# Optimization experiments

Measured on AMD Instinct MI355X. Metric: run time of the kernel, lower is better.

## Reference

```python
import jax, jax.numpy as jnp
import numpy as np

N = 50000
E = 800000
F_IN = 128


def _gat(h, src, dst, W, a_src, a_dst, bias, heads, out_ch, concat):
    n = h.shape[0]
    z = (h @ W.T).reshape(n, heads, out_ch)              # [N,H,C]
    alpha_s = jnp.sum(z * a_src, axis=-1)                # [N,H]
    alpha_d = jnp.sum(z * a_dst, axis=-1)                # [N,H]
    logits = jax.nn.leaky_relu(alpha_s[src] + alpha_d[dst], 0.2)  # [Etot,H]
    m = jax.ops.segment_max(logits, dst, num_segments=n)
    ex = jnp.exp(logits - m[dst])
    denom = jax.ops.segment_sum(ex, dst, num_segments=n)
    w = ex / (denom[dst] + 1e-16)                        # [Etot,H]
    agg = jax.ops.segment_sum(w[:, :, None] * z[src], dst, num_segments=n)  # [N,H,C]
    if concat:
        out = agg.reshape(n, heads * out_ch)
    else:
        out = agg.mean(axis=1)
    return out + bias


def setup_inputs() -> dict:
    key = jax.random.key(0)
    ks = jax.random.split(key, 16)
    s = lambda *sh: 1.0 / np.sqrt(sh[-1])
    inp = {
        "x": jax.random.normal(ks[0], (N, F_IN), jnp.float32),
        "edge_index": jax.random.randint(ks[1], (2, E), 0, N, jnp.int64),
        # GraphConv(no_node_features=128 -> 128, aggr='add')
        "W_rel": jax.random.normal(ks[2], (128, F_IN), jnp.float32) * s(128, F_IN),
        "b_rel": jnp.zeros((128,), jnp.float32),
        "W_root": jax.random.normal(ks[3], (128, F_IN), jnp.float32) * s(128, F_IN),
        # GATConv(128 -> 8, heads=8, concat) => 64
        "W1": jax.random.normal(ks[4], (64, 128), jnp.float32) * s(64, 128),
        "a1_src": jax.random.normal(ks[5], (8, 8), jnp.float32) * 0.35,
        "a1_dst": jax.random.normal(ks[6], (8, 8), jnp.float32) * 0.35,
        "b1": jnp.zeros((64,), jnp.float32),
        # GATConv(64 -> 64, heads=1, concat=False)
        "W2": jax.random.normal(ks[7], (64, 64), jnp.float32) * s(64, 64),
        "a2_src": jax.random.normal(ks[8], (1, 64), jnp.float32) * 0.125,
        "a2_dst": jax.random.normal(ks[9], (1, 64), jnp.float32) * 0.125,
        "b2": jnp.zeros((64,), jnp.float32),
        "Wr": jax.random.normal(ks[10], (1, 64), jnp.float32) * s(1, 64),
        "br": jnp.zeros((1,), jnp.float32),
    }
    return inp


def reference(x, edge_index, W_rel, b_rel, W_root, W1, a1_src, a1_dst, b1,
              W2, a2_src, a2_dst, b2, Wr, br):
    src, dst = edge_index[0], edge_index[1]
    # GraphConv, aggr='add': W_rel @ sum_{j in N(i)} x_j + b + W_root @ x_i
    nbr = jax.ops.segment_sum(x[src], dst, num_segments=N)
    h = nbr @ W_rel.T + b_rel + x @ W_root.T
    h = jax.nn.elu(h)
    # GATConv adds self-loops by default
    loop = jnp.arange(N, dtype=edge_index.dtype)
    src2 = jnp.concatenate([src, loop])
    dst2 = jnp.concatenate([dst, loop])
    h = _gat(h, src2, dst2, W1, a1_src, a1_dst, b1, heads=8, out_ch=8, concat=True)
    h = jax.nn.elu(h)
    h = _gat(h, src2, dst2, W2, a2_src, a2_dst, b2, heads=1, out_ch=64, concat=False)
    # final 'mean' aggregation over all nodes (single graph)
    g = jnp.mean(h, axis=0, keepdims=True)               # [1,64]
    return g @ Wr.T + br                                  # [1,1]
```

## Files before the change

kernel.cpp:

```cpp
#include <hip/hip_runtime.h>
#include <hip/hip_bf16.h>
#include <math.h>

#define N_NODES 50000
#define N_EDGES 800000
#define F_IN 128
#define NBUCK 391
#define EPB 4096
#define NBB 196

typedef __attribute__((ext_vector_type(8))) short bf16x8;
typedef __attribute__((ext_vector_type(4))) float f32x4;
typedef __attribute__((ext_vector_type(2))) float f32x2;
typedef unsigned long long ull;

__device__ __forceinline__ float elu_f(float x)   { return x > 0.f ? x : expm1f(x); }
__device__ __forceinline__ float lrelu_f(float x) { return x > 0.f ? x : 0.2f * x; }
__device__ __forceinline__ int   clampN(int v)    { return v < 0 ? 0 : (v >= N_NODES ? N_NODES - 1 : v); }
__device__ __forceinline__ float bits2f(unsigned int u) { union { unsigned int u; float f; } x; x.u = u; return x.f; }
__device__ __forceinline__ float bf2f(unsigned short s) { return bits2f(((unsigned int)s) << 16); }
__device__ __forceinline__ unsigned short f2bfbits(float f) {
    __hip_bfloat16 b = __float2bfloat16(f);
    return __builtin_bit_cast(unsigned short, b);
}
__device__ __forceinline__ unsigned int pack2(float lo, float hi) {
    return ((unsigned int)f2bfbits(hi) << 16) | f2bfbits(lo);
}

#define CAST_X_IDS (N_NODES * 32)
#define CAST_IDS (CAST_X_IDS + 32768 + 8192 + 4096)
#define CASTB ((CAST_IDS + 255) / 256)
__global__ __launch_bounds__(256) void k_prep(const int* __restrict__ dst,
                                              const float* __restrict__ x,
                                              const float* __restrict__ W_rel,
                                              const float* __restrict__ W_root,
                                              const float* __restrict__ W1,
                                              const float* __restrict__ W2,
                                              int* __restrict__ part,
                                              __hip_bfloat16* __restrict__ Abuf,
                                              unsigned int* __restrict__ x8,
                                              __hip_bfloat16* __restrict__ Wc,
                                              __hip_bfloat16* __restrict__ W1b,
                                              __hip_bfloat16* __restrict__ W2b,
                                              float* __restrict__ red,
                                              int* __restrict__ done) {
    __shared__ int hist[NBUCK];
    int tid = threadIdx.x;
    if (blockIdx.x < NBB) {
        for (int j = tid; j < NBUCK; j += 256) hist[j] = 0;
        __syncthreads();
        int base = blockIdx.x * EPB;
        #pragma unroll
        for (int t = 0; t < EPB / 256; ++t) {
            int e = base + t * 256 + tid;
            if (e < N_EDGES) atomicAdd(&hist[clampN(dst[e]) >> 7], 1);
        }
        __syncthreads();
        for (int j = tid; j < NBUCK; j += 256)
            part[(size_t)blockIdx.x * NBUCK + j] = hist[j];
    } else {
        if (blockIdx.x == NBB) {
            red[tid] = 0.f;
            if (tid == 0) done[0] = 0;
        }
        int id = (blockIdx.x - NBB) * 256 + tid;
        if (id < CAST_X_IDS) {
            int i = id >> 5, c4 = (id & 31) * 4;
            float4 v = *(const float4*)&x[(size_t)i * 128 + c4];
            ull p = (ull)f2bfbits(v.x) | ((ull)f2bfbits(v.y) << 16)
                  | ((ull)f2bfbits(v.z) << 32) | ((ull)f2bfbits(v.w) << 48);
            *(ull*)&Abuf[(size_t)i * 256 + 128 + c4] = p;
            int t = __builtin_amdgcn_cvt_pk_fp8_f32(v.x, v.y, 0, false);
            t = __builtin_amdgcn_cvt_pk_fp8_f32(v.z, v.w, t, true);
            x8[(size_t)i * 32 + (id & 31)] = (unsigned int)t;
        } else if (id < CAST_IDS) {
            int j = id - CAST_X_IDS;
            if (j < 32768) {
                int cc = j >> 8, k = j & 255;
                float v = (k < 128) ? W_rel[cc * 128 + k] : W_root[cc * 128 + (k - 128)];
                Wc[j] = __float2bfloat16(v);
            } else if (j < 32768 + 8192) {
                W1b[j - 32768] = __float2bfloat16(W1[j - 32768]);
            } else {
                W2b[j - 32768 - 8192] = __float2bfloat16(W2[j - 32768 - 8192]);
            }
        }
    }
}

__global__ __launch_bounds__(512) void k_bscan(const int* __restrict__ part,
                                               int* __restrict__ boff,
                                               int* __restrict__ bcur) {
    __shared__ int wsum[8];
    __shared__ int wbase[8];
    int tid = threadIdx.x;
    int lane = tid & 63, wid = tid >> 6;
    int v = 0;
    if (tid < NBUCK) {
        for (int b = 0; b < NBB; ++b) v += part[(size_t)b * NBUCK + tid];
    }
    int x = v;
    #pragma unroll
    for (int d = 1; d < 64; d <<= 1) {
        int t = __shfl_up(x, d, 64);
        if (lane >= d) x += t;
    }
    if (lane == 63) wsum[wid] = x;
    __syncthreads();
    if (tid == 0) {
        int b = 0;
        #pragma unroll
        for (int w = 0; w < 8; ++w) { wbase[w] = b; b += wsum[w]; }
    }
    __syncthreads();
    if (tid < NBUCK) {
        int e = wbase[wid] + x - v;
        boff[tid] = e;
        bcur[tid] = e;
    }
    if (tid == 0) boff[NBUCK] = N_EDGES;
}

__global__ __launch_bounds__(256) void k_bscatter(const int* __restrict__ src,
                                                  const int* __restrict__ dst,
                                                  int* __restrict__ bcur,
                                                  unsigned int* __restrict__ ebuf) {
    __shared__ int hist[NBUCK];
    __shared__ int hbase[NBUCK];
    int tid = threadIdx.x;
    for (int j = tid; j < NBUCK; j += 256) hist[j] = 0;
    __syncthreads();
    int base = blockIdx.x * EPB;
    unsigned int myP[EPB / 256]; int myB[EPB / 256], myR[EPB / 256];
    #pragma unroll
    for (int t = 0; t < EPB / 256; ++t) {
        int e = base + t * 256 + tid;
        if (e < N_EDGES) {
            int d = clampN(dst[e]);
            int s = clampN(src[e]);
            myP[t] = ((unsigned int)s << 7) | (unsigned int)(d & 127);
            myB[t] = d >> 7;
            myR[t] = atomicAdd(&hist[d >> 7], 1);
        } else myB[t] = -1;
    }
    __syncthreads();
    for (int j = tid; j < NBUCK; j += 256)
        if (hist[j]) hbase[j] = atomicAdd(&bcur[j], hist[j]);
    __syncthreads();
    #pragma unroll
    for (int t = 0; t < EPB / 256; ++t) {
        if (myB[t] >= 0) ebuf[hbase[myB[t]] + myR[t]] = myP[t];
    }
}

__global__ __launch_bounds__(256) void k_bfinal(const unsigned int* __restrict__ ebuf,
                                                const int* __restrict__ boff,
                                                int* __restrict__ offsets,
                                                int* __restrict__ csr) {
    __shared__ int cnt[128];
    __shared__ int cur[128];
    __shared__ int ws[4];
    int b = blockIdx.x;
    int tid = threadIdx.x;
    int node0 = b << 7;
    int k0 = boff[b], k1 = boff[b + 1];
    if (tid < 128) cnt[tid] = 0;
    __syncthreads();
    for (int k = k0 + tid; k < k1; k += 256)
        atomicAdd(&cnt[ebuf[k] & 127u], 1);
    __syncthreads();
    int lane = tid & 63;
    int v = (tid < 128) ? cnt[tid] : 0;
    int x = v;
    #pragma unroll
    for (int d = 1; d < 64; d <<= 1) {
        int t = __shfl_up(x, d, 64);
        if (lane >= d) x += t;
    }
    if (lane == 63) ws[tid >> 6] = x;
    __syncthreads();
    if (tid < 128) {
        int add = (tid >> 6) ? ws[0] : 0;
        int excl = k0 + add + x - v;
        cur[tid] = excl;
        int node = node0 + tid;
        if (node < N_NODES) offsets[node] = excl;
    }
    if (b == NBUCK - 1 && tid == 0) offsets[N_NODES] = N_EDGES;
    __syncthreads();
    for (int k = k0 + tid; k < k1; k += 256) {
        unsigned int e = ebuf[k];
        int r = atomicAdd(&cur[e & 127u], 1);
        csr[r] = (int)(e >> 7);
    }
}

__global__ __launch_bounds__(256) void k_gather(const unsigned int* __restrict__ x8,
                                                const int* __restrict__ offsets,
                                                const int* __restrict__ csr,
                                                ull* __restrict__ outNbr) {
    int i = blockIdx.x * 8 + (threadIdx.x >> 5);
    int l = threadIdx.x & 31;
    int k0 = offsets[i], k1 = offsets[i + 1];
    float a0 = 0.f, a1 = 0.f, a2 = 0.f, a3 = 0.f;
    for (int kb = k0; kb < k1; kb += 8) {
        int s[8]; int vm[8];
        #pragma unroll
        for (int j = 0; j < 8; ++j) {
            int kk = kb + j;
            vm[j] = kk < k1;
            s[j] = csr[vm[j] ? kk : k1 - 1];
        }
        unsigned int u[8];
        #pragma unroll
        for (int j = 0; j < 8; ++j) u[j] = x8[(size_t)s[j] * 32 + l];
        #pragma unroll
        for (int j = 0; j < 8; ++j) {
            if (vm[j]) {
                f32x2 lo = __builtin_amdgcn_cvt_pk_f32_fp8(u[j], false);
                f32x2 hi = __builtin_amdgcn_cvt_pk_f32_fp8(u[j], true);
                a0 += lo.x; a1 += lo.y; a2 += hi.x; a3 += hi.y;
            }
        }
    }
    outNbr[(size_t)i * 64 + l] = (ull)pack2(a0, a1) | ((ull)pack2(a2, a3) << 32);
}

__global__ __launch_bounds__(256) void k_gemm12(const __hip_bfloat16* __restrict__ A,
                                                const __hip_bfloat16* __restrict__ Wc,
                                                const float* __restrict__ bias,
                                                const __hip_bfloat16* __restrict__ W1b,
                                                const float* __restrict__ a_src,
                                                const float* __restrict__ a_dst,
                                                float* __restrict__ as_o,
                                                float* __restrict__ ad_o,
                                                unsigned int* __restrict__ z8) {
    __shared__ __align__(16) short smem[64 * 136];
    short (*sA)[40] = (short(*)[40])smem;
    short (*sW)[40] = (short(*)[40])(smem + 64 * 40);
    int tid = threadIdx.x;
    int lane = tid & 63, wave = tid >> 6;
    int quad = lane >> 4, l16 = lane & 15;
    int node0 = blockIdx.x * 64;
    int srow = tid >> 2, schk = (tid & 3) * 8;
    int ga = node0 + srow; if (ga >= N_NODES) ga = N_NODES - 1;
    const short* Ap = (const short*)A + (size_t)ga * 256 + schk;
    const short* Wp = (const short*)Wc;
    f32x4 acc[8];
    #pragma unroll
    for (int t = 0; t < 8; ++t) acc[t] = (f32x4){0.f, 0.f, 0.f, 0.f};
    for (int k0 = 0; k0 < 256; k0 += 32) {
        *(bf16x8*)&sA[srow][schk] = *(const bf16x8*)(Ap + k0);
        #pragma unroll
        for (int it = 0; it < 2; ++it) {
            int wrow = srow + it * 64;
            *(bf16x8*)&sW[wrow][schk] = *(const bf16x8*)(Wp + (size_t)wrow * 256 + k0 + schk);
        }
        __syncthreads();
        bf16x8 a = *(const bf16x8*)&sA[wave * 16 + l16][quad * 8];
        #pragma unroll
        for (int nt = 0; nt < 8; ++nt) {
            bf16x8 b = *(const bf16x8*)&sW[nt * 16 + l16][quad * 8];
            acc[nt] = __builtin_amdgcn_mfma_f32_16x16x32_bf16(a, b, acc[nt], 0, 0, 0);
        }
        __syncthreads();
    }
    #pragma unroll
    for (int nt = 0; nt < 8; ++nt) {
        int col = nt * 16 + l16;
        float bv = bias[col];
        #pragma unroll
        for (int r = 0; r < 4; ++r) {
            int row = wave * 16 + quad * 4 + r;
            smem[row * 136 + col] = (short)f2bfbits(elu_f(acc[nt][r] + bv));
        }
    }
    __syncthreads();
    f32x4 acc2[4];
    #pragma unroll
    for (int t = 0; t < 4; ++t) acc2[t] = (f32x4){0.f, 0.f, 0.f, 0.f};
    const short* W1p = (const short*)W1b;
    #pragma unroll
    for (int k0 = 0; k0 < 128; k0 += 32) {
        bf16x8 a = *(const bf16x8*)&smem[(wave * 16 + l16) * 136 + k0 + quad * 8];
        #pragma unroll
        for (int nt = 0; nt < 4; ++nt) {
            bf16x8 b = *(const bf16x8*)(W1p + (size_t)(nt * 16 + l16) * 128 + k0 + quad * 8);
            acc2[nt] = __builtin_amdgcn_mfma_f32_16x16x32_bf16(a, b, acc2[nt], 0, 0, 0);
        }
    }
    __syncthreads();
    #pragma unroll
    for (int nt = 0; nt < 4; ++nt) {
        int col = nt * 16 + l16;
        #pragma unroll
        for (int r = 0; r < 4; ++r) {
            int row = wave * 16 + quad * 4 + r;
            smem[row * 72 + col] = (short)f2bfbits(acc2[nt][r]);
        }
    }
    __syncthreads();
    int row = tid >> 2, chunk = tid & 3;
    int gi = node0 + row;
    float v[16];
    bf16x8 c0 = *(const bf16x8*)&smem[row * 72 + chunk * 16];
    bf16x8 c1 = *(const bf16x8*)&smem[row * 72 + chunk * 16 + 8];
    #pragma unroll
    for (int j = 0; j < 8; ++j) {
        v[j]     = bf2f((unsigned short)c0[j]);
        v[8 + j] = bf2f((unsigned short)c1[j]);
    }
    float ps0 = 0.f, pd0 = 0.f, ps1 = 0.f, pd1 = 0.f;
    #pragma unroll
    for (int j = 0; j < 8; ++j) {
        ps0 += v[j] * a_src[chunk * 16 + j];
        pd0 += v[j] * a_dst[chunk * 16 + j];
        ps1 += v[8 + j] * a_src[chunk * 16 + 8 + j];
        pd1 += v[8 + j] * a_dst[chunk * 16 + 8 + j];
    }
    if (gi < N_NODES) {
        as_o[(size_t)gi * 8 + 2 * chunk]     = ps0;
        as_o[(size_t)gi * 8 + 2 * chunk + 1] = ps1;
        ad_o[(size_t)gi * 8 + 2 * chunk]     = pd0;
        ad_o[(size_t)gi * 8 + 2 * chunk + 1] = pd1;
        #pragma unroll
        for (int wi = 0; wi < 4; ++wi) {
            int t = __builtin_amdgcn_cvt_pk_fp8_f32(v[4 * wi], v[4 * wi + 1], 0, false);
            t = __builtin_amdgcn_cvt_pk_fp8_f32(v[4 * wi + 2], v[4 * wi + 3], t, true);
            z8[(size_t)gi * 16 + chunk * 4 + wi] = (unsigned int)t;
        }
    }
}

__global__ __launch_bounds__(256) void k_gat1z2(const unsigned int* __restrict__ z8,
                                                const float* __restrict__ as1,
                                                const float* __restrict__ ad1,
                                                const float* __restrict__ b1,
                                                const int* __restrict__ offsets,
                                                const int* __restrict__ csr,
                                                const __hip_bfloat16* __restrict__ W2b,
                                                const float* __restrict__ a2s,
                                                const float* __restrict__ a2d,
                                                const float* __restrict__ Wr,
                                                float* __restrict__ as2,
                                                float* __restrict__ ad2,
                                                float* __restrict__ zr) {
    __shared__ __align__(16) short sH2[16 * 72];
    __shared__ __align__(16) short sZ2[16 * 72];
    int iloc = threadIdx.x >> 4;
    int i = blockIdx.x * 16 + iloc;
    int l = threadIdx.x & 15;
    int hd = l >> 1;
    int wh = l & 7, slot = l >> 3;
    int k0 = offsets[i], k1 = offsets[i + 1];
    float ad_h = ad1[(size_t)i * 8 + hd];
    float adw  = ad1[(size_t)i * 8 + wh];
    float e_self = __expf(lrelu_f(as1[(size_t)i * 8 + hd] + ad_h));
    unsigned int uz = z8[(size_t)i * 16 + l];
    f32x2 zlo = __builtin_amdgcn_cvt_pk_f32_fp8(uz, false);
    f32x2 zhi = __builtin_amdgcn_cvt_pk_f32_fp8(uz, true);
    float acc0 = e_self * zlo.x, acc1 = e_self * zlo.y;
    float acc2 = e_self * zhi.x, acc3 = e_self * zhi.y;
    float denp = 0.f;
    for (int kb = k0; kb < k1; kb += 8) {
        int sr[4]; float er[4];
        #pragma unroll
        for (int m = 0; m < 4; ++m) {
            int kk = kb + 2 * m + slot;
            bool v = kk < k1;
            int s = csr[v ? kk : k1 - 1];
            sr[m] = s;
            er[m] = v ? __expf(lrelu_f(as1[(size_t)s * 8 + wh] + adw)) : 0.f;
            denp += er[m];
        }
        int sj[8]; float ej[8]; unsigned int u[8];
        #pragma unroll
        for (int m = 0; m < 4; ++m) {
            #pragma unroll
            for (int sb = 0; sb < 2; ++sb) {
                sj[2 * m + sb] = __shfl(sr[m], sb * 8 + hd, 16);
                ej[2 * m + sb] = __shfl(er[m], sb * 8 + hd, 16);
            }
        }
        #pragma unroll
        for (int j = 0; j < 8; ++j) u[j] = z8[(size_t)sj[j] * 16 + l];
        #pragma unroll
        for (int j = 0; j < 8; ++j) {
            f32x2 alo = __builtin_amdgcn_cvt_pk_f32_fp8(u[j], false);
            f32x2 ahi = __builtin_amdgcn_cvt_pk_f32_fp8(u[j], true);
            acc0 += ej[j] * alo.x; acc1 += ej[j] * alo.y;
            acc2 += ej[j] * ahi.x; acc3 += ej[j] * ahi.y;
        }
    }
    denp += __shfl_xor(denp, 8, 16);
    float den = __shfl(denp, hd, 16) + e_self;
    float inv = 1.f / den;
    float r0 = elu_f(acc0 * inv + b1[4 * l + 0]);
    float r1 = elu_f(acc1 * inv + b1[4 * l + 1]);
    float r2 = elu_f(acc2 * inv + b1[4 * l + 2]);
    float r3 = elu_f(acc3 * inv + b1[4 * l + 3]);
    *(ull*)&sH2[iloc * 72 + 4 * l] = (ull)pack2(r0, r1) | ((ull)pack2(r2, r3) << 32);
    __syncthreads();
    int lane = threadIdx.x & 63, wave = threadIdx.x >> 6;
    int quad = lane >> 4, l16 = lane & 15;
    f32x4 accz = (f32x4){0.f, 0.f, 0.f, 0.f};
    const short* W2p = (const short*)W2b;
    #pragma unroll
    for (int kk0 = 0; kk0 < 64; kk0 += 32) {
        bf16x8 a = *(const bf16x8*)&sH2[l16 * 72 + kk0 + quad * 8];
        bf16x8 b = *(const bf16x8*)(W2p + (size_t)(wave * 16 + l16) * 64 + kk0 + quad * 8);
        accz = __builtin_amdgcn_mfma_f32_16x16x32_bf16(a, b, accz, 0, 0, 0);
    }
    #pragma unroll
    for (int r = 0; r < 4; ++r)
        sZ2[(quad * 4 + r) * 72 + wave * 16 + l16] = (short)f2bfbits(accz[r]);
    __syncthreads();
    ull pz = *(const ull*)&sZ2[iloc * 72 + 4 * l];
    float v0 = bf2f((unsigned short)(pz & 0xffff));
    float v1 = bf2f((unsigned short)((pz >> 16) & 0xffff));
    float v2 = bf2f((unsigned short)((pz >> 32) & 0xffff));
    float v3 = bf2f((unsigned short)(pz >> 48));
    float ps = v0 * a2s[4 * l + 0] + v1 * a2s[4 * l + 1] + v2 * a2s[4 * l + 2] + v3 * a2s[4 * l + 3];
    float pd = v0 * a2d[4 * l + 0] + v1 * a2d[4 * l + 1] + v2 * a2d[4 * l + 2] + v3 * a2d[4 * l + 3];
    float pr = v0 * Wr[4 * l + 0]  + v1 * Wr[4 * l + 1]  + v2 * Wr[4 * l + 2]  + v3 * Wr[4 * l + 3];
    #pragma unroll
    for (int d = 8; d >= 1; d >>= 1) {
        ps += __shfl_xor(ps, d, 16);
        pd += __shfl_xor(pd, d, 16);
        pr += __shfl_xor(pr, d, 16);
    }
    if (l == 0) { as2[i] = ps; ad2[i] = pd; zr[i] = pr; }
}

__global__ __launch_bounds__(256) void k_gat2s(const float* __restrict__ zr,
                                               const float* __restrict__ as2,
                                               const float* __restrict__ ad2,
                                               const int* __restrict__ offsets,
                                               const int* __restrict__ csr,
                                               const float* __restrict__ b2,
                                               const float* __restrict__ Wr,
                                               const float* __restrict__ br,
                                               float* __restrict__ red,
                                               int* __restrict__ done,
                                               float* __restrict__ out) {
    __shared__ float wsum[4];
    __shared__ int lastFlag;
    int tid = threadIdx.x;
    int n = blockIdx.x * 64 + (tid >> 2);
    int r = tid & 3;
    float c = 0.f;
    if (n < N_NODES) {
        int k0 = offsets[n], k1 = offsets[n + 1];
        float ad = ad2[n];
        float den = 0.f, num = 0.f;
        for (int k = k0 + r; k < k1; k += 4) {
            int s = csr[k];
            float e = __expf(lrelu_f(as2[s] + ad));
            den += e;
            num += e * zr[s];
        }
        den += __shfl_xor(den, 1, 64); den += __shfl_xor(den, 2, 64);
        num += __shfl_xor(num, 1, 64); num += __shfl_xor(num, 2, 64);
        if (r == 0) {
            float es = __expf(lrelu_f(as2[n] + ad));
            den += es;
            num += es * zr[n];
            c = num / den;
        }
    }
    #pragma unroll
    for (int d = 4; d <= 32; d <<= 1) c += __shfl_xor(c, d, 64);
    int lane = tid & 63, wave = tid >> 6;
    if (lane == 0) wsum[wave] = c;
    __syncthreads();
    if (tid == 0) {
        float s = wsum[0] + wsum[1] + wsum[2] + wsum[3];
        atomicAdd(&red[blockIdx.x & 255], s);
        __threadfence();
        int old = atomicAdd(done, 1);
        lastFlag = (old == (int)gridDim.x - 1);
    }
    __syncthreads();
    if (lastFlag) {
        __threadfence();
        if (tid < 64) {
            float rv = atomicAdd(&red[tid], 0.f) + atomicAdd(&red[tid + 64], 0.f)
                     + atomicAdd(&red[tid + 128], 0.f) + atomicAdd(&red[tid + 192], 0.f);
            float p = rv * (1.0f / N_NODES) + b2[tid] * Wr[tid];
            #pragma unroll
            for (int d = 32; d >= 1; d >>= 1) p += __shfl_xor(p, d, 64);
            if (tid == 0) out[0] = p + br[0];
        }
    }
}

extern "C" void kernel_launch(void* const* d_in, const int* in_sizes, int n_in,
                              void* d_out, int out_size, void* d_ws, size_t ws_size,
                              hipStream_t stream) {
    const float* x      = (const float*)d_in[0];
    const int*   edges  = (const int*)d_in[1];
    const float* W_rel  = (const float*)d_in[2];
    const float* b_rel  = (const float*)d_in[3];
    const float* W_root = (const float*)d_in[4];
    const float* W1     = (const float*)d_in[5];
    const float* a1s    = (const float*)d_in[6];
    const float* a1d    = (const float*)d_in[7];
    const float* b1     = (const float*)d_in[8];
    const float* W2     = (const float*)d_in[9];
    const float* a2s    = (const float*)d_in[10];
    const float* a2d    = (const float*)d_in[11];
    const float* b2     = (const float*)d_in[12];
    const float* Wr     = (const float*)d_in[13];
    const float* br     = (const float*)d_in[14];
    float* out = (float*)d_out;

    const int* src = edges;
    const int* dst = edges + N_EDGES;

    char* ws = (char*)d_ws;
    size_t p = 0;
    auto alloc = [&](size_t bytes) -> void* {
        void* r = ws + p;
        p = (p + bytes + 255) & ~(size_t)255;
        return r;
    };
    int*   part    = (int*)alloc((size_t)NBB * NBUCK * 4);
    int*   boff    = (int*)alloc((size_t)(NBUCK + 1) * 4);
    int*   bcur    = (int*)alloc((size_t)NBUCK * 4);
    unsigned int* ebuf = (unsigned int*)alloc((size_t)N_EDGES * 4);
    int*   offsets = (int*)alloc((size_t)(N_NODES + 1) * 4);
    int*   csr     = (int*)alloc((size_t)N_EDGES * 4);
    __hip_bfloat16* Abuf = (__hip_bfloat16*)alloc((size_t)N_NODES * 256 * 2);
    unsigned int* x8 = (unsigned int*)alloc((size_t)N_NODES * 32 * 4);
    __hip_bfloat16* Wc   = (__hip_bfloat16*)alloc((size_t)128 * 256 * 2);
    __hip_bfloat16* W1b  = (__hip_bfloat16*)alloc((size_t)64 * 128 * 2);
    __hip_bfloat16* W2b  = (__hip_bfloat16*)alloc((size_t)64 * 64 * 2);
    float* as1 = (float*)alloc((size_t)N_NODES * 8 * 4);
    float* ad1 = (float*)alloc((size_t)N_NODES * 8 * 4);
    float* as2 = (float*)alloc((size_t)N_NODES * 4);
    float* ad2 = (float*)alloc((size_t)N_NODES * 4);
    float* zr  = (float*)alloc((size_t)N_NODES * 4);
    unsigned int* z1e8 = (unsigned int*)alloc((size_t)N_NODES * 16 * 4);
    float* red = (float*)alloc(256 * 4);
    int*   done = (int*)alloc(4);

    const int MB   = (N_NODES + 63) / 64;
    const int NB8  = N_NODES / 8;
    const int NB16 = N_NODES / 16;

    k_prep    <<<NBB + CASTB, 256, 0, stream>>>(dst, x, W_rel, W_root, W1, W2,
                                                part, Abuf, x8, Wc, W1b, W2b, red, done);
    k_bscan   <<<1, 512, 0, stream>>>(part, boff, bcur);
    k_bscatter<<<NBB, 256, 0, stream>>>(src, dst, bcur, ebuf);
    k_bfinal  <<<NBUCK, 256, 0, stream>>>(ebuf, boff, offsets, csr);
    k_gather  <<<NB8, 256, 0, stream>>>(x8, offsets, csr, (ull*)Abuf);
    k_gemm12  <<<MB, 256, 0, stream>>>(Abuf, Wc, b_rel, W1b, a1s, a1d, as1, ad1, z1e8);
    k_gat1z2  <<<NB16, 256, 0, stream>>>(z1e8, as1, ad1, b1, offsets, csr,
                                         W2b, a2s, a2d, Wr, as2, ad2, zr);
    k_gat2s   <<<MB, 256, 0, stream>>>(zr, as2, ad2, offsets, csr, b2, Wr, br,
                                       red, done, out);
}
```

Baseline: 235.8 us.

## Use fixed-capacity buckets, drop histogram/scan, fuse neighbor gather into GEMM kernel

Replaces the histogram-plus-scan bucket sort with fixed-capacity buckets (CAP slots per 128-node bucket) addressed through a global counter, removing the histogram pass and the single-block scan kernel. Node offsets become int2 (begin,end) pairs because the CSR is no longer contiguous. The neighbor-sum gather now runs inside the GEMM kernel and writes straight into shared memory, so the bf16 neighbor half of Abuf is no longer written to and reread from global memory. The cost is a bucket that overflows if more than CAP edges land in it, and less parallelism in the fused gather phase.

```diff
diff --git a/kernel.cpp b/kernel.cpp
--- a/kernel.cpp
+++ b/kernel.cpp
@@ -8,6 +8,8 @@
 #define NBUCK 391
 #define EPB 4096
 #define NBB 196
+#define CAP 4096
+#define APITCH 264
 
 typedef __attribute__((ext_vector_type(8))) short bf16x8;
 typedef __attribute__((ext_vector_type(4))) float f32x4;
@@ -30,100 +32,53 @@
 #define CAST_X_IDS (N_NODES * 32)
 #define CAST_IDS (CAST_X_IDS + 32768 + 8192 + 4096)
 #define CASTB ((CAST_IDS + 255) / 256)
-__global__ __launch_bounds__(256) void k_prep(const int* __restrict__ dst,
-                                              const float* __restrict__ x,
+__global__ __launch_bounds__(256) void k_prep(const float* __restrict__ x,
                                               const float* __restrict__ W_rel,
                                               const float* __restrict__ W_root,
                                               const float* __restrict__ W1,
                                               const float* __restrict__ W2,
-                                              int* __restrict__ part,
                                               __hip_bfloat16* __restrict__ Abuf,
                                               unsigned int* __restrict__ x8,
                                               __hip_bfloat16* __restrict__ Wc,
                                               __hip_bfloat16* __restrict__ W1b,
                                               __hip_bfloat16* __restrict__ W2b,
+                                              int* __restrict__ gcount,
                                               float* __restrict__ red,
                                               int* __restrict__ done) {
-    __shared__ int hist[NBUCK];
     int tid = threadIdx.x;
-    if (blockIdx.x < NBB) {
-        for (int j = tid; j < NBUCK; j += 256) hist[j] = 0;
-        __syncthreads();
-        int base = blockIdx.x * EPB;
-        #pragma unroll
-        for (int t = 0; t < EPB / 256; ++t) {
-            int e = base + t * 256 + tid;
-            if (e < N_EDGES) atomicAdd(&hist[clampN(dst[e]) >> 7], 1);
-        }
-        __syncthreads();
-        for (int j = tid; j < NBUCK; j += 256)
-            part[(size_t)blockIdx.x * NBUCK + j] = hist[j];
-    } else {
-        if (blockIdx.x == NBB) {
-            red[tid] = 0.f;
-            if (tid == 0) done[0] = 0;
-        }
-        int id = (blockIdx.x - NBB) * 256 + tid;
-        if (id < CAST_X_IDS) {
-            int i = id >> 5, c4 = (id & 31) * 4;
-            float4 v = *(const float4*)&x[(size_t)i * 128 + c4];
-            ull p = (ull)f2bfbits(v.x) | ((ull)f2bfbits(v.y) << 16)
-                  | ((ull)f2bfbits(v.z) << 32) | ((ull)f2bfbits(v.w) << 48);
-            *(ull*)&Abuf[(size_t)i * 256 + 128 + c4] = p;
-            int t = __builtin_amdgcn_cvt_pk_fp8_f32(v.x, v.y, 0, false);
-            t = __builtin_amdgcn_cvt_pk_fp8_f32(v.z, v.w, t, true);
-            x8[(size_t)i * 32 + (id & 31)] = (unsigned int)t;
-        } else if (id < CAST_IDS) {
-            int j = id - CAST_X_IDS;
-            if (j < 32768) {
-                int cc = j >> 8, k = j & 255;
-                float v = (k < 128) ? W_rel[cc * 128 + k] : W_root[cc * 128 + (k - 128)];
-                Wc[j] = __float2bfloat16(v);
-            } else if (j < 32768 + 8192) {
-                W1b[j - 32768] = __float2bfloat16(W1[j - 32768]);
-            } else {
-                W2b[j - 32768 - 8192] = __float2bfloat16(W2[j - 32768 - 8192]);
-            }
-        }
-    }
-}
-
-__global__ __launch_bounds__(512) void k_bscan(const int* __restrict__ part,
-                                               int* __restrict__ boff,
-                                               int* __restrict__ bcur) {
-    __shared__ int wsum[8];
-    __shared__ int wbase[8];
-    int tid = threadIdx.x;
-    int lane = tid & 63, wid = tid >> 6;
-    int v = 0;
-    if (tid < NBUCK) {
-        for (int b = 0; b < NBB; ++b) v += part[(size_t)b * NBUCK + tid];
-    }
-    int x = v;
-    #pragma unroll
-    for (int d = 1; d < 64; d <<= 1) {
-        int t = __shfl_up(x, d, 64);
-        if (lane >= d) x += t;
-    }
-    if (lane == 63) wsum[wid] = x;
-    __syncthreads();
-    if (tid == 0) {
-        int b = 0;
-        #pragma unroll
-        for (int w = 0; w < 8; ++w) { wbase[w] = b; b += wsum[w]; }
-    }
-    __syncthreads();
-    if (tid < NBUCK) {
-        int e = wbase[wid] + x - v;
-        boff[tid] = e;
-        bcur[tid] = e;
-    }
-    if (tid == 0) boff[NBUCK] = N_EDGES;
+    if (blockIdx.x == 0) {
+        red[tid] = 0.f;
+        if (tid < NBUCK) gcount[tid] = 0;
+        if (tid + 256 < NBUCK) gcount[tid + 256] = 0;
+        if (tid == 0) done[0] = 0;
+    }
+    int id = blockIdx.x * 256 + tid;
+    if (id < CAST_X_IDS) {
+        int i = id >> 5, c4 = (id & 31) * 4;
+        float4 v = *(const float4*)&x[(size_t)i * 128 + c4];
+        ull p = (ull)f2bfbits(v.x) | ((ull)f2bfbits(v.y) << 16)
+              | ((ull)f2bfbits(v.z) << 32) | ((ull)f2bfbits(v.w) << 48);
+        *(ull*)&Abuf[(size_t)i * 128 + c4] = p;
+        int t = __builtin_amdgcn_cvt_pk_fp8_f32(v.x, v.y, 0, false);
+        t = __builtin_amdgcn_cvt_pk_fp8_f32(v.z, v.w, t, true);
+        x8[(size_t)i * 32 + (id & 31)] = (unsigned int)t;
+    } else if (id < CAST_IDS) {
+        int j = id - CAST_X_IDS;
+        if (j < 32768) {
+            int cc = j >> 8, k = j & 255;
+            float v = (k < 128) ? W_rel[cc * 128 + k] : W_root[cc * 128 + (k - 128)];
+            Wc[j] = __float2bfloat16(v);
+        } else if (j < 32768 + 8192) {
+            W1b[j - 32768] = __float2bfloat16(W1[j - 32768]);
+        } else {
+            W2b[j - 32768 - 8192] = __float2bfloat16(W2[j - 32768 - 8192]);
+        }
+    }
 }
 
 __global__ __launch_bounds__(256) void k_bscatter(const int* __restrict__ src,
                                                   const int* __restrict__ dst,
-                                                  int* __restrict__ bcur,
+                                                  int* __restrict__ gcount,
                                                   unsigned int* __restrict__ ebuf) {
     __shared__ int hist[NBUCK];
     __shared__ int hbase[NBUCK];
@@ -145,7 +100,7 @@
     }
     __syncthreads();
     for (int j = tid; j < NBUCK; j += 256)
-        if (hist[j]) hbase[j] = atomicAdd(&bcur[j], hist[j]);
+        if (hist[j]) hbase[j] = j * CAP + atomicAdd(&gcount[j], hist[j]);
     __syncthreads();
     #pragma unroll
     for (int t = 0; t < EPB / 256; ++t) {
@@ -154,8 +109,8 @@
 }
 
 __global__ __launch_bounds__(256) void k_bfinal(const unsigned int* __restrict__ ebuf,
-                                                const int* __restrict__ boff,
-                                                int* __restrict__ offsets,
+                                                const int* __restrict__ gcount,
+                                                int2* __restrict__ offs,
                                                 int* __restrict__ csr) {
     __shared__ int cnt[128];
     __shared__ int cur[128];
@@ -163,7 +118,7 @@
     int b = blockIdx.x;
     int tid = threadIdx.x;
     int node0 = b << 7;
-    int k0 = boff[b], k1 = boff[b + 1];
+    int k0 = b * CAP, k1 = k0 + gcount[b];
     if (tid < 128) cnt[tid] = 0;
     __syncthreads();
     for (int k = k0 + tid; k < k1; k += 256)
@@ -184,9 +139,8 @@
         int excl = k0 + add + x - v;
         cur[tid] = excl;
         int node = node0 + tid;
-        if (node < N_NODES) offsets[node] = excl;
-    }
-    if (b == NBUCK - 1 && tid == 0) offsets[N_NODES] = N_EDGES;
+        if (node < N_NODES) offs[node] = make_int2(excl, excl + v);
+    }
     __syncthreads();
     for (int k = k0 + tid; k < k1; k += 256) {
         unsigned int e = ebuf[k];
@@ -195,38 +149,10 @@
     }
 }
 
-__global__ __launch_bounds__(256) void k_gather(const unsigned int* __restrict__ x8,
-                                                const int* __restrict__ offsets,
+__global__ __launch_bounds__(256) void k_gemm12(const unsigned int* __restrict__ x8,
+                                                const int2* __restrict__ offs,
                                                 const int* __restrict__ csr,
-                                                ull* __restrict__ outNbr) {
-    int i = blockIdx.x * 8 + (threadIdx.x >> 5);
-    int l = threadIdx.x & 31;
-    int k0 = offsets[i], k1 = offsets[i + 1];
-    float a0 = 0.f, a1 = 0.f, a2 = 0.f, a3 = 0.f;
-    for (int kb = k0; kb < k1; kb += 8) {
-        int s[8]; int vm[8];
-        #pragma unroll
-        for (int j = 0; j < 8; ++j) {
-            int kk = kb + j;
-            vm[j] = kk < k1;
-            s[j] = csr[vm[j] ? kk : k1 - 1];
-        }
-        unsigned int u[8];
-        #pragma unroll
-        for (int j = 0; j < 8; ++j) u[j] = x8[(size_t)s[j] * 32 + l];
-        #pragma unroll
-        for (int j = 0; j < 8; ++j) {
-            if (vm[j]) {
-                f32x2 lo = __builtin_amdgcn_cvt_pk_f32_fp8(u[j], false);
-                f32x2 hi = __builtin_amdgcn_cvt_pk_f32_fp8(u[j], true);
-                a0 += lo.x; a1 += lo.y; a2 += hi.x; a3 += hi.y;
-            }
-        }
-    }
-    outNbr[(size_t)i * 64 + l] = (ull)pack2(a0, a1) | ((ull)pack2(a2, a3) << 32);
-}
-
-__global__ __launch_bounds__(256) void k_gemm12(const __hip_bfloat16* __restrict__ A,
+                                                const __hip_bfloat16* __restrict__ Ax,
                                                 const __hip_bfloat16* __restrict__ Wc,
                                                 const float* __restrict__ bias,
                                                 const __hip_bfloat16* __restrict__ W1b,
@@ -235,29 +161,69 @@
                                                 float* __restrict__ as_o,
                                                 float* __restrict__ ad_o,
                                                 unsigned int* __restrict__ z8) {
-    __shared__ __align__(16) short smem[64 * 136];
-    short (*sA)[40] = (short(*)[40])smem;
-    short (*sW)[40] = (short(*)[40])(smem + 64 * 40);
+    __shared__ __align__(16) short smem[64 * APITCH + 128 * 40];
+    short* sAF = smem;
+    short (*sW)[40] = (short(*)[40])(smem + 64 * APITCH);
     int tid = threadIdx.x;
     int lane = tid & 63, wave = tid >> 6;
     int quad = lane >> 4, l16 = lane & 15;
     int node0 = blockIdx.x * 64;
+
+    {
+        int l = tid & 31;
+        for (int r8 = 0; r8 < 8; ++r8) {
+            int rloc = r8 * 8 + (tid >> 5);
+            int i = node0 + rloc;
+            bool valid = i < N_NODES;
+            int2 oe = valid ? offs[i] : make_int2(0, 0);
+            int k0 = oe.x, k1 = oe.y;
+            float a0 = 0.f, a1 = 0.f, a2 = 0.f, a3 = 0.f;
+            for (int kb = k0; kb < k1; kb += 8) {
+                int s[8]; int vm[8];
+                #pragma unroll
+                for (int j = 0; j < 8; ++j) {
+                    int kk = kb + j;
+                    vm[j] = kk < k1;
+                    s[j] = csr[vm[j] ? kk : k1 - 1];
+                }
+                unsigned int u[8];
+                #pragma unroll
+                for (int j = 0; j < 8; ++j) u[j] = x8[(size_t)s[j] * 32 + l];
+                #pragma unroll
+                for (int j = 0; j < 8; ++j) {
+                    if (vm[j]) {
+                        f32x2 lo = __builtin_amdgcn_cvt_pk_f32_fp8(u[j], false);
+                        f32x2 hi = __builtin_amdgcn_cvt_pk_f32_fp8(u[j], true);
+                        a0 += lo.x; a1 += lo.y; a2 += hi.x; a3 += hi.y;
+                    }
+                }
+            }
+            *(ull*)&sAF[rloc * APITCH + 4 * l] = (ull)pack2(a0, a1) | ((ull)pack2(a2, a3) << 32);
+        }
+    }
+    {
+        int row = tid >> 2, c32 = (tid & 3) * 32;
+        int gx = node0 + row; if (gx >= N_NODES) gx = N_NODES - 1;
+        const short* xp = (const short*)Ax + (size_t)gx * 128 + c32;
+        #pragma unroll
+        for (int q = 0; q < 4; ++q)
+            *(bf16x8*)&sAF[row * APITCH + 128 + c32 + q * 8] = *(const bf16x8*)(xp + q * 8);
+    }
+    __syncthreads();
+
     int srow = tid >> 2, schk = (tid & 3) * 8;
-    int ga = node0 + srow; if (ga >= N_NODES) ga = N_NODES - 1;
-    const short* Ap = (const short*)A + (size_t)ga * 256 + schk;
     const short* Wp = (const short*)Wc;
     f32x4 acc[8];
     #pragma unroll
     for (int t = 0; t < 8; ++t) acc[t] = (f32x4){0.f, 0.f, 0.f, 0.f};
     for (int k0 = 0; k0 < 256; k0 += 32) {
-        *(bf16x8*)&sA[srow][schk] = *(const bf16x8*)(Ap + k0);
         #pragma unroll
         for (int it = 0; it < 2; ++it) {
             int wrow = srow + it * 64;
             *(bf16x8*)&sW[wrow][schk] = *(const bf16x8*)(Wp + (size_t)wrow * 256 + k0 + schk);
         }
         __syncthreads();
-        bf16x8 a = *(const bf16x8*)&sA[wave * 16 + l16][quad * 8];
+        bf16x8 a = *(const bf16x8*)&sAF[(wave * 16 + l16) * APITCH + k0 + quad * 8];
         #pragma unroll
         for (int nt = 0; nt < 8; ++nt) {
             bf16x8 b = *(const bf16x8*)&sW[nt * 16 + l16][quad * 8];
@@ -272,7 +238,7 @@
         #pragma unroll
         for (int r = 0; r < 4; ++r) {
             int row = wave * 16 + quad * 4 + r;
-            smem[row * 136 + col] = (short)f2bfbits(elu_f(acc[nt][r] + bv));
+            sAF[row * APITCH + col] = (short)f2bfbits(elu_f(acc[nt][r] + bv));
         }
     }
     __syncthreads();
@@ -282,7 +248,7 @@
     const short* W1p = (const short*)W1b;
     #pragma unroll
     for (int k0 = 0; k0 < 128; k0 += 32) {
-        bf16x8 a = *(const bf16x8*)&smem[(wave * 16 + l16) * 136 + k0 + quad * 8];
+        bf16x8 a = *(const bf16x8*)&sAF[(wave * 16 + l16) * APITCH + k0 + quad * 8];
         #pragma unroll
         for (int nt = 0; nt < 4; ++nt) {
             bf16x8 b = *(const bf16x8*)(W1p + (size_t)(nt * 16 + l16) * 128 + k0 + quad * 8);
@@ -336,7 +302,7 @@
                                                 const float* __restrict__ as1,
                                                 const float* __restrict__ ad1,
                                                 const float* __restrict__ b1,
-                                                const int* __restrict__ offsets,
+                                                const int2* __restrict__ offs,
                                                 const int* __restrict__ csr,
                                                 const __hip_bfloat16* __restrict__ W2b,
                                                 const float* __restrict__ a2s,
@@ -352,7 +318,8 @@
     int l = threadIdx.x & 15;
     int hd = l >> 1;
     int wh = l & 7, slot = l >> 3;
-    int k0 = offsets[i], k1 = offsets[i + 1];
+    int2 oe = offs[i];
+    int k0 = oe.x, k1 = oe.y;
     float ad_h = ad1[(size_t)i * 8 + hd];
     float adw  = ad1[(size_t)i * 8 + wh];
     float e_self = __expf(lrelu_f(as1[(size_t)i * 8 + hd] + ad_h));
@@ -435,7 +402,7 @@
 __global__ __launch_bounds__(256) void k_gat2s(const float* __restrict__ zr,
                                                const float* __restrict__ as2,
                                                const float* __restrict__ ad2,
-                                               const int* __restrict__ offsets,
+                                               const int2* __restrict__ offs,
                                                const int* __restrict__ csr,
                                                const float* __restrict__ b2,
                                                const float* __restrict__ Wr,
@@ -450,10 +417,10 @@
     int r = tid & 3;
     float c = 0.f;
     if (n < N_NODES) {
-        int k0 = offsets[n], k1 = offsets[n + 1];
+        int2 oe = offs[n];
         float ad = ad2[n];
         float den = 0.f, num = 0.f;
-        for (int k = k0 + r; k < k1; k += 4) {
+        for (int k = oe.x + r; k < oe.y; k += 4) {
             int s = csr[k];
             float e = __expf(lrelu_f(as2[s] + ad));
             den += e;
@@ -524,13 +491,11 @@
         p = (p + bytes + 255) & ~(size_t)255;
         return r;
     };
-    int*   part    = (int*)alloc((size_t)NBB * NBUCK * 4);
-    int*   boff    = (int*)alloc((size_t)(NBUCK + 1) * 4);
-    int*   bcur    = (int*)alloc((size_t)NBUCK * 4);
-    unsigned int* ebuf = (unsigned int*)alloc((size_t)N_EDGES * 4);
-    int*   offsets = (int*)alloc((size_t)(N_NODES + 1) * 4);
-    int*   csr     = (int*)alloc((size_t)N_EDGES * 4);
-    __hip_bfloat16* Abuf = (__hip_bfloat16*)alloc((size_t)N_NODES * 256 * 2);
+    unsigned int* ebuf = (unsigned int*)alloc((size_t)NBUCK * CAP * 4);
+    int2*  offs    = (int2*)alloc((size_t)N_NODES * 8);
+    int*   csr     = (int*)alloc((size_t)NBUCK * CAP * 4);
+    int*   gcount  = (int*)alloc((size_t)NBUCK * 4);
+    __hip_bfloat16* Abuf = (__hip_bfloat16*)alloc((size_t)N_NODES * 128 * 2);
     unsigned int* x8 = (unsigned int*)alloc((size_t)N_NODES * 32 * 4);
     __hip_bfloat16* Wc   = (__hip_bfloat16*)alloc((size_t)128 * 256 * 2);
     __hip_bfloat16* W1b  = (__hip_bfloat16*)alloc((size_t)64 * 128 * 2);
@@ -545,18 +510,16 @@
     int*   done = (int*)alloc(4);
 
     const int MB   = (N_NODES + 63) / 64;
-    const int NB8  = N_NODES / 8;
     const int NB16 = N_NODES / 16;
 
-    k_prep    <<<NBB + CASTB, 256, 0, stream>>>(dst, x, W_rel, W_root, W1, W2,
-                                                part, Abuf, x8, Wc, W1b, W2b, red, done);
-    k_bscan   <<<1, 512, 0, stream>>>(part, boff, bcur);
-    k_bscatter<<<NBB, 256, 0, stream>>>(src, dst, bcur, ebuf);
-    k_bfinal  <<<NBUCK, 256, 0, stream>>>(ebuf, boff, offsets, csr);
-    k_gather  <<<NB8, 256, 0, stream>>>(x8, offsets, csr, (ull*)Abuf);
-    k_gemm12  <<<MB, 256, 0, stream>>>(Abuf, Wc, b_rel, W1b, a1s, a1d, as1, ad1, z1e8);
-    k_gat1z2  <<<NB16, 256, 0, stream>>>(z1e8, as1, ad1, b1, offsets, csr,
+    k_prep    <<<CASTB, 256, 0, stream>>>(x, W_rel, W_root, W1, W2,
+                                          Abuf, x8, Wc, W1b, W2b, gcount, red, done);
+    k_bscatter<<<NBB, 256, 0, stream>>>(src, dst, gcount, ebuf);
+    k_bfinal  <<<NBUCK, 256, 0, stream>>>(ebuf, gcount, offs, csr);
+    k_gemm12  <<<MB, 256, 0, stream>>>(x8, offs, csr, Abuf, Wc, b_rel, W1b,
+                                       a1s, a1d, as1, ad1, z1e8);
+    k_gat1z2  <<<NB16, 256, 0, stream>>>(z1e8, as1, ad1, b1, offs, csr,
                                          W2b, a2s, a2d, Wr, as2, ad2, zr);
-    k_gat2s   <<<MB, 256, 0, stream>>>(zr, as2, ad2, offsets, csr, b2, Wr, br,
+    k_gat2s   <<<MB, 256, 0, stream>>>(zr, as2, ad2, offs, csr, b2, Wr, br,
                                        red, done, out);
 }
```

Measured after the change: 259.3 us. 10.0% more time.
